# Optimization experiments

Measured on AMD Instinct MI355X. Metric: run time of the kernel, lower is better.

The kernel has to match this reference:

```python
import jax, jax.numpy as jnp
import numpy as np
from jax import lax

CLASSES = 6
R = 8            # zoom_factor
FEAT = 32        # DUC loops i,j in range(32)
OUT_PAD = 304    # DUC hardcodes zeros(b,6,304,304)
IMG = 256        # original image H=W -> final bilinear resize target
BN_EPS = 1e-5
DN = ('NCHW', 'OIHW', 'NCHW')


def _duc(x):
    # x: [B, classes*r*r, H', W'] ; original loop only reads top-left 32x32
    x = x[:, :, :FEAT, :FEAT]
    B = x.shape[0]
    # channel order in original: view(b, classes, r*r) -> (classes, r, r)
    y = x.reshape(B, CLASSES, R, R, FEAT, FEAT)
    y = y.transpose(0, 1, 4, 2, 5, 3).reshape(B, CLASSES, FEAT * R, FEAT * R)  # [B,6,256,256]
    pad = OUT_PAD - FEAT * R
    return jnp.pad(y, ((0, 0), (0, 0), (0, pad), (0, pad)))  # zeros ring like torch.zeros buffer


def _bilinear_align_corners(x, oh, ow):
    b, c, h, w = x.shape
    ys = jnp.linspace(0.0, h - 1.0, oh)
    xs = jnp.linspace(0.0, w - 1.0, ow)
    y0 = jnp.floor(ys).astype(jnp.int32)
    x0 = jnp.floor(xs).astype(jnp.int32)
    y1 = jnp.minimum(y0 + 1, h - 1)
    x1 = jnp.minimum(x0 + 1, w - 1)
    wy = (ys - y0)[None, None, :, None]
    wx = (xs - x0)[None, None, None, :]
    rows = x[:, :, y0, :] * (1.0 - wy) + x[:, :, y1, :] * wy          # [b,c,oh,w]
    out = rows[:, :, :, x0] * (1.0 - wx) + rows[:, :, :, x1] * wx     # [b,c,oh,ow]
    return out


def setup_inputs() -> dict:
    key = jax.random.key(0)
    ks = jax.random.split(key, 8)
    x = jax.random.normal(ks[0], (16, 5632, 32, 32), jnp.float32)
    w1 = jax.random.normal(ks[1], (512, 5632, 1, 1), jnp.float32) * 0.02
    gamma = 1.0 + 0.1 * jax.random.normal(ks[2], (512,), jnp.float32)
    beta = 0.1 * jax.random.normal(ks[3], (512,), jnp.float32)
    mean = 0.1 * jax.random.normal(ks[4], (512,), jnp.float32)
    var = jax.random.uniform(ks[5], (512,), jnp.float32, 0.5, 1.5)
    w2 = jax.random.normal(ks[6], (CLASSES * R * R, 512, 1, 1), jnp.float32) * 0.02
    b2 = jax.random.normal(ks[7], (CLASSES * R * R,), jnp.float32) * 0.02
    return {'x': x, 'w1': w1, 'gamma': gamma, 'beta': beta, 'mean': mean, 'var': var, 'w2': w2, 'b2': b2}


def reference(x, w1, gamma, beta, mean, var, w2, b2):
    # cls head: 1x1 conv with padding=1 (quirk in source) -> 34x34 map
    h = lax.conv_general_dilated(x, w1, (1, 1), ((1, 1), (1, 1)), dimension_numbers=DN)
    inv = lax.rsqrt(var + BN_EPS)
    h = (h - mean[None, :, None, None]) * (inv * gamma)[None, :, None, None] + beta[None, :, None, None]
    h = jax.nn.relu(h)  # Dropout2d is identity at inference
    h = lax.conv_general_dilated(h, w2, (1, 1), ((0, 0), (0, 0)), dimension_numbers=DN)
    h = h + b2[None, :, None, None]            # [B,384,34,34]
    h = _duc(h)                                # [B,6,304,304]
    h = jax.nn.softmax(h, axis=1)
    return _bilinear_align_corners(h, IMG, IMG)  # [B,6,256,256]
```

## Files before the change

kernel.cpp:

```cpp
#include <hip/hip_runtime.h>
#include <hip/hip_bf16.h>
#include <stdint.h>

typedef float f32x4 __attribute__((ext_vector_type(4)));
typedef short s16x8 __attribute__((ext_vector_type(8)));
typedef unsigned short u16;

__device__ __forceinline__ u16 f2bf(float f) {
  uint32_t u = __float_as_uint(f);
  u = (u + 0x7fffu + ((u >> 16) & 1u)) >> 16;
  return (u16)u;
}

__device__ __forceinline__ short cvt_bf(float f) {
  union { __hip_bfloat16 h; short s; } c;
  c.h = __float2bfloat16(f);
  return c.s;
}

__device__ __forceinline__ void wg_barrier_lds() {
  __builtin_amdgcn_sched_barrier(0);
  asm volatile("s_waitcnt lgkmcnt(0)" ::: "memory");
  __builtin_amdgcn_s_barrier();
  __builtin_amdgcn_sched_barrier(0);
}

__global__ void k_params(const float* __restrict__ gamma, const float* __restrict__ beta,
                         const float* __restrict__ mean, const float* __restrict__ var,
                         float* __restrict__ bnS, float* __restrict__ bnT) {
  int i = threadIdx.x;
  if (i < 512) {
    float s = gamma[i] * rsqrtf(var[i] + 1e-5f);
    bnS[i] = s;
    bnT[i] = beta[i] - mean[i] * s;
  }
}

__global__ void k_convert(const float* __restrict__ in, u16* __restrict__ out, int n4) {
  int i = blockIdx.x * blockDim.x + threadIdx.x;
  if (i < n4) {
    float4 v = ((const float4*)in)[i];
    ushort4 o;
    o.x = f2bf(v.x); o.y = f2bf(v.y); o.z = f2bf(v.z); o.w = f2bf(v.w);
    ((ushort4*)out)[i] = o;
  }
}

__global__ void k_border2(const float* __restrict__ w2, const float* __restrict__ b2,
                          const float* __restrict__ bnT, float* __restrict__ border2) {
  int o = blockIdx.x;
  int l = threadIdx.x;
  float s = 0.f;
  for (int j = 0; j < 8; ++j) {
    int c = l + 64 * j;
    s += w2[o * 512 + c] * fmaxf(bnT[c], 0.f);
  }
  for (int off = 32; off > 0; off >>= 1) s += __shfl_down(s, off, 64);
  if (l == 0) border2[o] = s + b2[o];
}

template <int MODE>
__global__ __launch_bounds__(256, 2) void k_gemm1(
    const float* __restrict__ X, const u16* __restrict__ Bw,
    const float* __restrict__ bnS, const float* __restrict__ bnT,
    u16* __restrict__ H, float* __restrict__ P) {
  const int K = 5632;
  const int NT = (MODE == 1) ? 88 : 176;
  __shared__ __align__(16) u16 sA[2][128 * 40];
  __shared__ __align__(16) u16 sB[2][4096];
  int id = blockIdx.x;
  int inner = id & 511;
  int kh = (MODE == 1) ? (id >> 9) : 0;
  int kbase = kh * 2816;
  int li = (inner & 7) * 64 + (inner >> 3);
  int nt = li & 3;
  int mt = li >> 2;
  int t = threadIdx.x;
  int l = t & 63, w = t >> 6;
  int wm = w >> 1, wn = w & 1;

  auto swz = [](int u) { int m = u >> 2, g = u & 3; return (m * 4 + (g ^ ((m >> 1) & 3))) * 8; };
  int wo0 = swz(t), wo1 = swz(t + 256);
  const u16* gB0 = Bw + (size_t)(nt * 128 + (t >> 2)) * K + kbase + (t & 3) * 8;
  const u16* gB1 = gB0 + (size_t)64 * K;

  int m0 = (w >> 1) * 64 + 2 * (l & 31);
  int kh2 = w & 1, kq = l >> 5;
  int bidx = mt >> 3, p0 = (mt & 7) * 128;
  const float* gA = X + (size_t)bidx * (5632ull * 1024)
                      + (size_t)(kbase + kh2 * 16 + kq * 8) * 1024 + p0 + m0;
  int aoff = m0 * 40 + kh2 * 16 + kq * 8;

  int offA[4], offB[4];
#pragma unroll
  for (int f = 0; f < 4; ++f) {
    int m = wm * 64 + f * 16 + (l & 15);
    offA[f] = m * 40 + (l >> 4) * 8;
    int n = wn * 64 + f * 16 + (l & 15);
    int g = l >> 4;
    offB[f] = (n * 4 + (g ^ ((n >> 1) & 3))) * 8;
  }

  f32x4 acc[4][4] = {};

  float2 xa0, xa1, xa2, xa3, xa4, xa5, xa6, xa7;
  float2 xb0, xb1, xb2, xb3, xb4, xb5, xb6, xb7;
  s16x8 ra0, ra1, rb0, rb1;

#define LOADX(s)                                                        \
  do {                                                                  \
    (x##s##0) = *(const float2*)(gA);                                   \
    (x##s##1) = *(const float2*)(gA + 1024);                            \
    (x##s##2) = *(const float2*)(gA + 2048);                            \
    (x##s##3) = *(const float2*)(gA + 3072);                            \
    (x##s##4) = *(const float2*)(gA + 4096);                            \
    (x##s##5) = *(const float2*)(gA + 5120);                            \
    (x##s##6) = *(const float2*)(gA + 6144);                            \
    (x##s##7) = *(const float2*)(gA + 7168);                            \
    (r##s##0) = *(const s16x8*)gB0;                                     \
    (r##s##1) = *(const s16x8*)gB1;                                     \
  } while (0)

#define ADVX()                                                          \
  do { gA += 32 * 1024; gB0 += 32; gB1 += 32; } while (0)

#define STAGEX(s, bufA, bufB)                                           \
  do {                                                                  \
    s16x8 lo_ = {cvt_bf((x##s##0).x), cvt_bf((x##s##1).x),              \
                 cvt_bf((x##s##2).x), cvt_bf((x##s##3).x),              \
                 cvt_bf((x##s##4).x), cvt_bf((x##s##5).x),              \
                 cvt_bf((x##s##6).x), cvt_bf((x##s##7).x)};             \
    s16x8 hi_ = {cvt_bf((x##s##0).y), cvt_bf((x##s##1).y),              \
                 cvt_bf((x##s##2).y), cvt_bf((x##s##3).y),              \
                 cvt_bf((x##s##4).y), cvt_bf((x##s##5).y),              \
                 cvt_bf((x##s##6).y), cvt_bf((x##s##7).y)};             \
    *(s16x8*)((bufA) + aoff) = lo_;                                     \
    *(s16x8*)((bufA) + aoff + 40) = hi_;                                \
    *(s16x8*)((bufB) + wo0) = (r##s##0);                                \
    *(s16x8*)((bufB) + wo1) = (r##s##1);                                \
  } while (0)

#define COMPUTEX(bufA, bufB)                                            \
  do {                                                                  \
    s16x8 af[4], bfr[4];                                                \
    _Pragma("unroll") for (int f = 0; f < 4; ++f) {                     \
      af[f] = *(const s16x8*)((bufA) + offA[f]);                        \
      bfr[f] = *(const s16x8*)((bufB) + offB[f]);                       \
    }                                                                   \
    _Pragma("unroll") for (int ii = 0; ii < 4; ++ii)                    \
      _Pragma("unroll") for (int j = 0; j < 4; ++j)                     \
        acc[ii][j] = __builtin_amdgcn_mfma_f32_16x16x32_bf16(           \
            af[ii], bfr[j], acc[ii][j], 0, 0, 0);                       \
  } while (0)

  LOADX(a);
  STAGEX(a, sA[0], sB[0]);
  ADVX();
  LOADX(b);

  for (int i = 0; i < NT; i += 2) {
    wg_barrier_lds();
    if (i + 2 < NT) { ADVX(); LOADX(a); }
    COMPUTEX(sA[0], sB[0]);
    STAGEX(b, sA[1], sB[1]);
    wg_barrier_lds();
    if (i + 3 < NT) { ADVX(); LOADX(b); }
    COMPUTEX(sA[1], sB[1]);
    if (i + 2 < NT) STAGEX(a, sA[0], sB[0]);
  }
#undef LOADX
#undef ADVX
#undef STAGEX
#undef COMPUTEX

  int mb = mt * 128 + wm * 64;
  int nbase = nt * 128 + wn * 64;
  if (MODE == 0) {
#pragma unroll
    for (int j = 0; j < 4; ++j) {
      int n_g = nbase + j * 16 + (l & 15);
      float s = bnS[n_g], tt = bnT[n_g];
#pragma unroll
      for (int i = 0; i < 4; ++i)
#pragma unroll
        for (int r = 0; r < 4; ++r) {
          int m_g = mb + i * 16 + (l >> 4) * 4 + r;
          float v = fmaxf(acc[i][j][r] * s + tt, 0.f);
          H[(size_t)m_g * 512 + n_g] = f2bf(v);
        }
    }
  } else {
    float* Pd = P + (size_t)kh * (16384ull * 512);
#pragma unroll
    for (int j = 0; j < 4; ++j) {
      int n_g = nbase + j * 16 + (l & 15);
#pragma unroll
      for (int i = 0; i < 4; ++i)
#pragma unroll
        for (int r = 0; r < 4; ++r) {
          int m_g = mb + i * 16 + (l >> 4) * 4 + r;
          Pd[(size_t)m_g * 512 + n_g] = acc[i][j][r];
        }
    }
  }
}

__global__ __launch_bounds__(256) void k_combine(
    const float* __restrict__ P, const float* __restrict__ bnS,
    const float* __restrict__ bnT, u16* __restrict__ H) {
  int i = blockIdx.x * 256 + threadIdx.x;
  const float4 a = ((const float4*)P)[i];
  const float4 b = ((const float4*)(P + 16384ull * 512))[i];
  int n0 = (i * 4) & 511;
  float4 s = *(const float4*)(bnS + n0);
  float4 tt = *(const float4*)(bnT + n0);
  ushort4 o;
  o.x = (u16)(unsigned short)cvt_bf(fmaxf((a.x + b.x) * s.x + tt.x, 0.f));
  o.y = (u16)(unsigned short)cvt_bf(fmaxf((a.y + b.y) * s.y + tt.y, 0.f));
  o.z = (u16)(unsigned short)cvt_bf(fmaxf((a.z + b.z) * s.z + tt.z, 0.f));
  o.w = (u16)(unsigned short)cvt_bf(fmaxf((a.w + b.w) * s.w + tt.w, 0.f));
  ((ushort4*)H)[i] = o;
}

__global__ __launch_bounds__(256, 2) void k_gemm2(
    const u16* __restrict__ A, const u16* __restrict__ B,
    const float* __restrict__ b2, float* __restrict__ C) {
  const int K = 512;
  __shared__ __align__(16) u16 sA[4096];
  __shared__ __align__(16) u16 sB[4096];
  int nb = gridDim.x;
  int id = blockIdx.x;
  int li = (id & 7) * (nb >> 3) + (id >> 3);
  int nt = li % 3;
  int mt = li / 3;
  int t = threadIdx.x;
  int l = t & 63, w = t >> 6;
  int wm = w >> 1, wn = w & 1;

  auto swz = [](int u) { int m = u >> 2, g = u & 3; return (m * 4 + (g ^ ((m >> 1) & 3))) * 8; };
  int wo0 = swz(t), wo1 = swz(t + 256);

  const u16* gA0 = A + (size_t)(mt * 128 + (t >> 2)) * K + (t & 3) * 8;
  const u16* gA1 = gA0 + (size_t)64 * K;
  const u16* gB0 = B + (size_t)(nt * 128 + (t >> 2)) * K + (t & 3) * 8;
  const u16* gB1 = gB0 + (size_t)64 * K;

  int offA[4], offB[4];
#pragma unroll
  for (int f = 0; f < 4; ++f) {
    int g = l >> 4;
    int m = wm * 64 + f * 16 + (l & 15);
    offA[f] = (m * 4 + (g ^ ((m >> 1) & 3))) * 8;
    int n = wn * 64 + f * 16 + (l & 15);
    offB[f] = (n * 4 + (g ^ ((n >> 1) & 3))) * 8;
  }

  f32x4 acc[4][4] = {};

  s16x8 rA0 = *(const s16x8*)gA0;
  s16x8 rA1 = *(const s16x8*)gA1;
  s16x8 rB0 = *(const s16x8*)gB0;
  s16x8 rB1 = *(const s16x8*)gB1;

  for (int k0 = 0; k0 < K; k0 += 32) {
    *(s16x8*)(sA + wo0) = rA0;
    *(s16x8*)(sA + wo1) = rA1;
    *(s16x8*)(sB + wo0) = rB0;
    *(s16x8*)(sB + wo1) = rB1;
    wg_barrier_lds();
    if (k0 + 32 < K) {
      gA0 += 32; gA1 += 32; gB0 += 32; gB1 += 32;
      rA0 = *(const s16x8*)gA0;
      rA1 = *(const s16x8*)gA1;
      rB0 = *(const s16x8*)gB0;
      rB1 = *(const s16x8*)gB1;
    }
    s16x8 af[4], bf[4];
#pragma unroll
    for (int f = 0; f < 4; ++f) {
      af[f] = *(const s16x8*)(sA + offA[f]);
      bf[f] = *(const s16x8*)(sB + offB[f]);
    }
#pragma unroll
    for (int i = 0; i < 4; ++i)
#pragma unroll
      for (int j = 0; j < 4; ++j)
        acc[i][j] = __builtin_amdgcn_mfma_f32_16x16x32_bf16(af[i], bf[j], acc[i][j], 0, 0, 0);
    wg_barrier_lds();
  }

  int mb = mt * 128 + wm * 64;
  int nbase = nt * 128 + wn * 64;
#pragma unroll
  for (int j = 0; j < 4; ++j) {
    int n_g = nbase + j * 16 + (l & 15);
    float bias = b2[n_g];
#pragma unroll
    for (int i = 0; i < 4; ++i)
#pragma unroll
      for (int r = 0; r < 4; ++r) {
        int m_g = mb + i * 16 + (l >> 4) * 4 + r;
        C[(size_t)m_g * 384 + n_g] = acc[i][j][r] + bias;
      }
  }
}

__global__ __launch_bounds__(256) void k_out(const float* __restrict__ c2,
                                             const float* __restrict__ border2,
                                             float* __restrict__ out) {
  int b = blockIdx.x >> 8;
  int oy = blockIdx.x & 255;
  int ox = threadIdx.x;
  const float SCL = 303.0f / 255.0f;
  float ys = oy * SCL, xs = ox * SCL;
  int y0 = (int)ys; if (y0 > 303) y0 = 303;
  int x0 = (int)xs; if (x0 > 303) x0 = 303;
  float wy = ys - (float)y0, wx = xs - (float)x0;
  int y1 = y0 + 1; if (y1 > 303) y1 = 303;
  int x1 = x0 + 1; if (x1 > 303) x1 = 303;
  int syA[2] = {y0, y1};
  int sxA[2] = {x0, x1};
  float wyA[2] = {1.f - wy, wy};
  float wxA[2] = {1.f - wx, wx};
  float acc[6] = {0.f, 0.f, 0.f, 0.f, 0.f, 0.f};
#pragma unroll
  for (int cy = 0; cy < 2; ++cy) {
#pragma unroll
    for (int cx = 0; cx < 2; ++cx) {
      float wgt = wyA[cy] * wxA[cx];
      int sy = syA[cy], sx = sxA[cx];
      if (sy >= 256 || sx >= 256) {
        float p = wgt * (1.f / 6.f);
#pragma unroll
        for (int c = 0; c < 6; ++c) acc[c] += p;
      } else {
        int i = sy >> 3, j = sx >> 3;
        int sub = ((sy & 7) << 3) | (sx & 7);
        const float* src;
        if (i == 0 || j == 0)
          src = border2 + sub;
        else
          src = c2 + (size_t)((b << 10) + ((i - 1) << 5) + (j - 1)) * 384 + sub;
        float l0 = src[0],   l1 = src[64],  l2 = src[128];
        float l3 = src[192], l4 = src[256], l5 = src[320];
        float mx = fmaxf(fmaxf(fmaxf(l0, l1), fmaxf(l2, l3)), fmaxf(l4, l5));
        float e0 = __expf(l0 - mx), e1 = __expf(l1 - mx), e2 = __expf(l2 - mx);
        float e3 = __expf(l3 - mx), e4 = __expf(l4 - mx), e5 = __expf(l5 - mx);
        float ssum = e0 + e1 + e2 + e3 + e4 + e5;
        float r = wgt / ssum;
        acc[0] += e0 * r; acc[1] += e1 * r; acc[2] += e2 * r;
        acc[3] += e3 * r; acc[4] += e4 * r; acc[5] += e5 * r;
      }
    }
  }
  size_t base = ((size_t)b * 6) << 16;
  int pix = (oy << 8) | ox;
#pragma unroll
  for (int c = 0; c < 6; ++c) out[base + ((size_t)c << 16) + pix] = acc[c];
}

extern "C" void kernel_launch(void* const* d_in, const int* in_sizes, int n_in,
                              void* d_out, int out_size, void* d_ws, size_t ws_size,
                              hipStream_t stream) {
  const float* x     = (const float*)d_in[0];
  const float* w1    = (const float*)d_in[1];
  const float* gamma = (const float*)d_in[2];
  const float* beta  = (const float*)d_in[3];
  const float* mean  = (const float*)d_in[4];
  const float* var   = (const float*)d_in[5];
  const float* w2    = (const float*)d_in[6];
  const float* b2    = (const float*)d_in[7];
  float* out = (float*)d_out;

  char* ws = (char*)d_ws;
  size_t off = 0;
  auto alloc = [&](size_t bytes) -> char* {
    char* p = ws + off;
    off = (off + bytes + 255) & ~(size_t)255;
    return p;
  };
  u16*   w1bf    = (u16*)alloc(512ull * 5632 * 2);
  u16*   w2bf    = (u16*)alloc(384ull * 512 * 2);
  float* bnS     = (float*)alloc(512 * 4);
  float* bnT     = (float*)alloc(512 * 4);
  float* border2 = (float*)alloc(384 * 4);
  u16*   h       = (u16*)alloc(16384ull * 512 * 2);
  float* c2      = (float*)alloc(16384ull * 384 * 4);

  const size_t PB = 16384ull * 512 * 4;
  bool split = (off + 2 * PB + 4096 <= ws_size);
  float* P = split ? (float*)alloc(2 * PB) : nullptr;

  k_params<<<dim3(1), dim3(512), 0, stream>>>(gamma, beta, mean, var, bnS, bnT);
  k_convert<<<dim3(2816), dim3(256), 0, stream>>>(w1, w1bf, 512 * 5632 / 4);
  k_convert<<<dim3(192), dim3(256), 0, stream>>>(w2, w2bf, 384 * 512 / 4);
  k_border2<<<dim3(384), dim3(64), 0, stream>>>(w2, b2, bnT, border2);

  if (split) {
    k_gemm1<1><<<dim3(1024), dim3(256), 0, stream>>>(x, w1bf, bnS, bnT, h, P);
    k_combine<<<dim3(8192), dim3(256), 0, stream>>>(P, bnS, bnT, h);
  } else {
    k_gemm1<0><<<dim3(512), dim3(256), 0, stream>>>(x, w1bf, bnS, bnT, h, nullptr);
  }
  k_gemm2<<<dim3(128 * 3), dim3(256), 0, stream>>>(h, w2bf, b2, c2);
  k_out<<<dim3(16 * 256), dim3(256), 0, stream>>>(c2, border2, out);
}
```

Measured before the change: 264.5 us.

## Widen GEMM1 blocks to 512 threads with 2x4 wave grid and XOR-swizzled A tile

```diff
diff --git a/kernel.cpp b/kernel.cpp
--- a/kernel.cpp
+++ b/kernel.cpp
@@ -4,6 +4,7 @@
 
 typedef float f32x4 __attribute__((ext_vector_type(4)));
 typedef short s16x8 __attribute__((ext_vector_type(8)));
+typedef short s16x4 __attribute__((ext_vector_type(4)));
 typedef unsigned short u16;
 
 __device__ __forceinline__ u16 f2bf(float f) {
@@ -60,13 +61,13 @@
 }
 
 template <int MODE>
-__global__ __launch_bounds__(256, 2) void k_gemm1(
+__global__ __launch_bounds__(512, 4) void k_gemm1(
     const float* __restrict__ X, const u16* __restrict__ Bw,
     const float* __restrict__ bnS, const float* __restrict__ bnT,
     u16* __restrict__ H, float* __restrict__ P) {
   const int K = 5632;
   const int NT = (MODE == 1) ? 88 : 176;
-  __shared__ __align__(16) u16 sA[2][128 * 40];
+  __shared__ __align__(16) u16 sA[2][4096];
   __shared__ __align__(16) u16 sB[2][4096];
   int id = blockIdx.x;
   int inner = id & 511;
@@ -77,35 +78,28 @@
   int mt = li >> 2;
   int t = threadIdx.x;
   int l = t & 63, w = t >> 6;
-  int wm = w >> 1, wn = w & 1;
-
-  auto swz = [](int u) { int m = u >> 2, g = u & 3; return (m * 4 + (g ^ ((m >> 1) & 3))) * 8; };
-  int wo0 = swz(t), wo1 = swz(t + 256);
-  const u16* gB0 = Bw + (size_t)(nt * 128 + (t >> 2)) * K + kbase + (t & 3) * 8;
-  const u16* gB1 = gB0 + (size_t)64 * K;
-
-  int m0 = (w >> 1) * 64 + 2 * (l & 31);
-  int kh2 = w & 1, kq = l >> 5;
+  int wm = w >> 2, wn = w & 3;
+
+  int woB;
+  { int n = t >> 2, g = t & 3; woB = (n * 4 + (g ^ ((n >> 1) & 3))) * 8; }
+  const u16* gB = Bw + (size_t)(nt * 128 + (t >> 2)) * K + kbase + (t & 3) * 8;
+
+  int m0 = 2 * (t >> 3);
+  int kc = t & 7;
   int bidx = mt >> 3, p0 = (mt & 7) * 128;
   const float* gA = X + (size_t)bidx * (5632ull * 1024)
-                      + (size_t)(kbase + kh2 * 16 + kq * 8) * 1024 + p0 + m0;
-  int aoff = m0 * 40 + kh2 * 16 + kq * 8;
-
-  int offA[4], offB[4];
-#pragma unroll
-  for (int f = 0; f < 4; ++f) {
-    int m = wm * 64 + f * 16 + (l & 15);
-    offA[f] = m * 40 + (l >> 4) * 8;
-    int n = wn * 64 + f * 16 + (l & 15);
-    int g = l >> 4;
-    offB[f] = (n * 4 + (g ^ ((n >> 1) & 3))) * 8;
-  }
-
-  f32x4 acc[4][4] = {};
-
-  float2 xa0, xa1, xa2, xa3, xa4, xa5, xa6, xa7;
-  float2 xb0, xb1, xb2, xb3, xb4, xb5, xb6, xb7;
-  s16x8 ra0, ra1, rb0, rb1;
+                      + (size_t)(kbase + kc * 4) * 1024 + p0 + m0;
+  int aoff = m0 * 32 + ((kc >> 1) ^ ((m0 >> 1) & 3)) * 8 + (kc & 1) * 4;
+
+  int xorb = ((l & 15) >> 1) & 3;
+  int offA0 = (wm * 64 + (l & 15)) * 32 + ((l >> 4) ^ xorb) * 8;
+  int offB0 = (wn * 32 + (l & 15)) * 32 + ((l >> 4) ^ xorb) * 8;
+
+  f32x4 acc[4][2] = {};
+
+  float2 xa0, xa1, xa2, xa3;
+  float2 xb0, xb1, xb2, xb3;
+  s16x8 raB, rbB;
 
 #define LOADX(s)                                                        \
   do {                                                                  \
@@ -113,44 +107,39 @@
     (x##s##1) = *(const float2*)(gA + 1024);                            \
     (x##s##2) = *(const float2*)(gA + 2048);                            \
     (x##s##3) = *(const float2*)(gA + 3072);                            \
-    (x##s##4) = *(const float2*)(gA + 4096);                            \
-    (x##s##5) = *(const float2*)(gA + 5120);                            \
-    (x##s##6) = *(const float2*)(gA + 6144);                            \
-    (x##s##7) = *(const float2*)(gA + 7168);                            \
-    (r##s##0) = *(const s16x8*)gB0;                                     \
-    (r##s##1) = *(const s16x8*)gB1;                                     \
+    (r##s##B) = *(const s16x8*)gB;                                      \
   } while (0)
 
 #define ADVX()                                                          \
-  do { gA += 32 * 1024; gB0 += 32; gB1 += 32; } while (0)
+  do { gA += 32 * 1024; gB += 32; } while (0)
 
 #define STAGEX(s, bufA, bufB)                                           \
   do {                                                                  \
-    s16x8 lo_ = {cvt_bf((x##s##0).x), cvt_bf((x##s##1).x),              \
-                 cvt_bf((x##s##2).x), cvt_bf((x##s##3).x),              \
-                 cvt_bf((x##s##4).x), cvt_bf((x##s##5).x),              \
-                 cvt_bf((x##s##6).x), cvt_bf((x##s##7).x)};             \
-    s16x8 hi_ = {cvt_bf((x##s##0).y), cvt_bf((x##s##1).y),              \
-                 cvt_bf((x##s##2).y), cvt_bf((x##s##3).y),              \
-                 cvt_bf((x##s##4).y), cvt_bf((x##s##5).y),              \
-                 cvt_bf((x##s##6).y), cvt_bf((x##s##7).y)};             \
-    *(s16x8*)((bufA) + aoff) = lo_;                                     \
-    *(s16x8*)((bufA) + aoff + 40) = hi_;                                \
-    *(s16x8*)((bufB) + wo0) = (r##s##0);                                \
-    *(s16x8*)((bufB) + wo1) = (r##s##1);                                \
+    s16x4 lo_ = {cvt_bf((x##s##0).x), cvt_bf((x##s##1).x),              \
+                 cvt_bf((x##s##2).x), cvt_bf((x##s##3).x)};             \
+    s16x4 hi_ = {cvt_bf((x##s##0).y), cvt_bf((x##s##1).y),              \
+                 cvt_bf((x##s##2).y), cvt_bf((x##s##3).y)};             \
+    *(s16x4*)((bufA) + aoff) = lo_;                                     \
+    *(s16x4*)((bufA) + aoff + 32) = hi_;                                \
+    *(s16x8*)((bufB) + woB) = (r##s##B);                                \
   } while (0)
 
 #define COMPUTEX(bufA, bufB)                                            \
   do {                                                                  \
-    s16x8 af[4], bfr[4];                                                \
-    _Pragma("unroll") for (int f = 0; f < 4; ++f) {                     \
-      af[f] = *(const s16x8*)((bufA) + offA[f]);                        \
-      bfr[f] = *(const s16x8*)((bufB) + offB[f]);                       \
-    }                                                                   \
-    _Pragma("unroll") for (int ii = 0; ii < 4; ++ii)                    \
-      _Pragma("unroll") for (int j = 0; j < 4; ++j)                     \
-        acc[ii][j] = __builtin_amdgcn_mfma_f32_16x16x32_bf16(           \
-            af[ii], bfr[j], acc[ii][j], 0, 0, 0);                       \
+    s16x8 af0 = *(const s16x8*)((bufA) + offA0);                        \
+    s16x8 af1 = *(const s16x8*)((bufA) + offA0 + 512);                  \
+    s16x8 af2 = *(const s16x8*)((bufA) + offA0 + 1024);                 \
+    s16x8 af3 = *(const s16x8*)((bufA) + offA0 + 1536);                 \
+    s16x8 bf0 = *(const s16x8*)((bufB) + offB0);                        \
+    s16x8 bf1 = *(const s16x8*)((bufB) + offB0 + 512);                  \
+    acc[0][0] = __builtin_amdgcn_mfma_f32_16x16x32_bf16(af0, bf0, acc[0][0], 0, 0, 0); \
+    acc[0][1] = __builtin_amdgcn_mfma_f32_16x16x32_bf16(af0, bf1, acc[0][1], 0, 0, 0); \
+    acc[1][0] = __builtin_amdgcn_mfma_f32_16x16x32_bf16(af1, bf0, acc[1][0], 0, 0, 0); \
+    acc[1][1] = __builtin_amdgcn_mfma_f32_16x16x32_bf16(af1, bf1, acc[1][1], 0, 0, 0); \
+    acc[2][0] = __builtin_amdgcn_mfma_f32_16x16x32_bf16(af2, bf0, acc[2][0], 0, 0, 0); \
+    acc[2][1] = __builtin_amdgcn_mfma_f32_16x16x32_bf16(af2, bf1, acc[2][1], 0, 0, 0); \
+    acc[3][0] = __builtin_amdgcn_mfma_f32_16x16x32_bf16(af3, bf0, acc[3][0], 0, 0, 0); \
+    acc[3][1] = __builtin_amdgcn_mfma_f32_16x16x32_bf16(af3, bf1, acc[3][1], 0, 0, 0); \
   } while (0)
 
   LOADX(a);
@@ -174,11 +163,11 @@
 #undef COMPUTEX
 
   int mb = mt * 128 + wm * 64;
-  int nbase = nt * 128 + wn * 64;
+  int nb0 = nt * 128 + wn * 32;
   if (MODE == 0) {
 #pragma unroll
-    for (int j = 0; j < 4; ++j) {
-      int n_g = nbase + j * 16 + (l & 15);
+    for (int j = 0; j < 2; ++j) {
+      int n_g = nb0 + j * 16 + (l & 15);
       float s = bnS[n_g], tt = bnT[n_g];
 #pragma unroll
       for (int i = 0; i < 4; ++i)
@@ -192,8 +181,8 @@
   } else {
     float* Pd = P + (size_t)kh * (16384ull * 512);
 #pragma unroll
-    for (int j = 0; j < 4; ++j) {
-      int n_g = nbase + j * 16 + (l & 15);
+    for (int j = 0; j < 2; ++j) {
+      int n_g = nb0 + j * 16 + (l & 15);
 #pragma unroll
       for (int i = 0; i < 4; ++i)
 #pragma unroll
@@ -397,10 +386,10 @@
   k_border2<<<dim3(384), dim3(64), 0, stream>>>(w2, b2, bnT, border2);
 
   if (split) {
-    k_gemm1<1><<<dim3(1024), dim3(256), 0, stream>>>(x, w1bf, bnS, bnT, h, P);
+    k_gemm1<1><<<dim3(1024), dim3(512), 0, stream>>>(x, w1bf, bnS, bnT, h, P);
     k_combine<<<dim3(8192), dim3(256), 0, stream>>>(P, bnS, bnT, h);
   } else {
-    k_gemm1<0><<<dim3(512), dim3(256), 0, stream>>>(x, w1bf, bnS, bnT, h, nullptr);
+    k_gemm1<0><<<dim3(512), dim3(512), 0, stream>>>(x, w1bf, bnS, bnT, h, nullptr);
   }
   k_gemm2<<<dim3(128 * 3), dim3(256), 0, stream>>>(h, w2bf, b2, c2);
   k_out<<<dim3(16 * 256), dim3(256), 0, stream>>>(c2, border2, out);
```

New measurement: 432.7 us. 1.64x slower.
